# Optimization experiments

Hardware: AMD Instinct MI355X
Metric: run time of the kernel (lower is better)

## Reference

```python
import jax, jax.numpy as jnp
import numpy as np

N_NODES = 50000


def setup_inputs() -> dict:
    key = jax.random.key(0)
    ks = jax.random.split(key, 9)
    d = 256
    E = 800000
    inp = {
        "x": jax.random.normal(ks[0], (N_NODES, d), dtype=jnp.float32),
        "edge_index": jax.random.randint(ks[1], (2, E), 0, N_NODES, dtype=jnp.int64),
    }
    # 3 GCNConv layers, each: weight [in, out] and bias [out] (Glorot-ish scale)
    scale = 1.0 / np.sqrt(d)
    for i in range(3):
        inp[f"W{i+1}"] = jax.random.normal(ks[2 + 2 * i], (d, d), dtype=jnp.float32) * scale
        inp[f"b{i+1}"] = jnp.zeros((d,), dtype=jnp.float32)
    return inp


def _gcn_conv(h, src, dst, norm, W, b, n_nodes):
    # linear transform then normalized gather-scatter aggregation
    h = h @ W                                   # [N, out]
    msg = h[src] * norm[:, None]                # [E+N, out]
    out = jax.ops.segment_sum(msg, dst, num_segments=n_nodes)
    return out + b


def reference(x, edge_index, W1, b1, W2, b2, W3, b3):
    n = x.shape[0]
    loop = jnp.arange(n, dtype=edge_index.dtype)
    src = jnp.concatenate([edge_index[0], loop])  # add self-loops
    dst = jnp.concatenate([edge_index[1], loop])
    # symmetric normalization: deg^{-1/2}[src] * deg^{-1/2}[dst]
    deg = jax.ops.segment_sum(jnp.ones_like(dst, dtype=x.dtype), dst, num_segments=n)
    dinv = jnp.where(deg > 0, jax.lax.rsqrt(deg), 0.0)
    norm = dinv[src] * dinv[dst]

    h = _gcn_conv(x, src, dst, norm, W1, b1, n)
    h = jax.nn.relu(h)
    h = _gcn_conv(h, src, dst, norm, W2, b2, n)
    h = jax.nn.relu(h)
    h = _gcn_conv(h, src, dst, norm, W3, b3, n)
    return h
```

## Files before the change

kernel.cpp:

```cpp
#include <hip/hip_runtime.h>
#include <math.h>


using bf16x8  = __attribute__((ext_vector_type(8))) short;
using ushort4v = __attribute__((ext_vector_type(4))) unsigned short;
using f32x4   = __attribute__((ext_vector_type(4))) float;
using half4   = __attribute__((ext_vector_type(4))) _Float16;

__device__ inline unsigned short f2bf(float v) {
    union { float f; unsigned u; } x; x.f = v;
    unsigned r = x.u + 0x7fff + ((x.u >> 16) & 1);
    return (unsigned short)(r >> 16);
}
__device__ inline float bf2f(unsigned short b) {
    union { float f; unsigned u; } x; x.u = ((unsigned)b) << 16;
    return x.f;
}
__device__ inline unsigned short f2h_bits(float v) {
    _Float16 h = (_Float16)v;
    union { _Float16 h; unsigned short u; } c; c.h = h;
    return c.u;
}


__global__ void hist_kernel(const int* __restrict__ dst, int E, int* __restrict__ cnt) {
    int e = blockIdx.x * blockDim.x + threadIdx.x;
    if (e < E) atomicAdd(&cnt[dst[e]], 1);
}

__global__ void scan_block_kernel(const int* __restrict__ in, int n,
                                  int* __restrict__ out, int* __restrict__ bsums) {
    __shared__ int s[256];
    int t = threadIdx.x;
    int i = blockIdx.x * 256 + t;
    s[t] = (i < n) ? in[i] : 0;
    __syncthreads();
    for (int off = 1; off < 256; off <<= 1) {
        int addv = (t >= off) ? s[t - off] : 0;
        __syncthreads();
        s[t] += addv;
        __syncthreads();
    }
    if (i < n) out[i] = s[t];
    if (t == 255) bsums[blockIdx.x] = s[255];
}

__global__ void scan_sums_kernel(int* __restrict__ bsums, int nb) {
    __shared__ int s[256];
    int t = threadIdx.x;
    s[t] = (t < nb) ? bsums[t] : 0;
    __syncthreads();
    for (int off = 1; off < 256; off <<= 1) {
        int addv = (t >= off) ? s[t - off] : 0;
        __syncthreads();
        s[t] += addv;
        __syncthreads();
    }
    if (t < nb) bsums[t] = s[t];
}

__global__ void scan_add_dinv_kernel(int* __restrict__ scn, int n, const int* __restrict__ bsums,
                                     const int* __restrict__ cnt, float* __restrict__ dinv,
                                     int* __restrict__ cursor) {
    int i = blockIdx.x * 256 + threadIdx.x;
    if (i < n) {
        int s = scn[i] + (blockIdx.x > 0 ? bsums[blockIdx.x - 1] : 0);
        scn[i] = s;
        int c = cnt[i];
        dinv[i] = rsqrtf((float)(c + 1));
        cursor[i] = s - c;
    }
}

__global__ void scatter_kernel(const int* __restrict__ src, const int* __restrict__ dst, int E,
                               const float* __restrict__ dinv, int* __restrict__ cursor,
                               int* __restrict__ ssrc, float* __restrict__ snorm) {
    int e = blockIdx.x * blockDim.x + threadIdx.x;
    if (e < E) {
        int s = src[e], d0 = dst[e];
        int pos = atomicAdd(&cursor[d0], 1);
        ssrc[pos] = s;
        snorm[pos] = dinv[s] * dinv[d0];
    }
}

__global__ __launch_bounds__(256) void wsplit3_kernel(const float* __restrict__ Wa,
                                                      const float* __restrict__ Wb,
                                                      const float* __restrict__ Wc,
                                                      unsigned short* __restrict__ Wsp) {
    __shared__ float t[64][65];
    int w = blockIdx.z;
    const float* W = (w == 0) ? Wa : (w == 1) ? Wb : Wc;
    int k0 = blockIdx.x * 64, n0 = blockIdx.y * 64;
    int tid = threadIdx.x;
    int r = tid >> 6, c = tid & 63;
#pragma unroll
    for (int i = 0; i < 16; ++i) {
        int kk = i * 4 + r;
        t[kk][c] = W[(size_t)(k0 + kk) * 256 + n0 + c];
    }
    __syncthreads();
    unsigned short* Hi = Wsp + (size_t)w * 131072;
    unsigned short* Lo = Hi + 65536;
#pragma unroll
    for (int i = 0; i < 16; ++i) {
        int nn = i * 4 + r;
        float v = t[c][nn];
        unsigned short h = f2bf(v);
        unsigned short l2 = f2bf(v - bf2f(h));
        Hi[(size_t)(n0 + nn) * 256 + k0 + c] = h;
        Lo[(size_t)(n0 + nn) * 256 + k0 + c] = l2;
    }
}

__global__ void xsplit_kernel(const float* __restrict__ in, unsigned short* __restrict__ hi,
                              unsigned short* __restrict__ lo, int total4) {
    int i = blockIdx.x * blockDim.x + threadIdx.x;
    int stride = gridDim.x * blockDim.x;
    for (; i < total4; i += stride) {
        float4 v = ((const float4*)in)[i];
        ushort4v h, l;
        h[0] = f2bf(v.x); l[0] = f2bf(v.x - bf2f(h[0]));
        h[1] = f2bf(v.y); l[1] = f2bf(v.y - bf2f(h[1]));
        h[2] = f2bf(v.z); l[2] = f2bf(v.z - bf2f(h[2]));
        h[3] = f2bf(v.w); l[3] = f2bf(v.w - bf2f(h[3]));
        ((ushort4v*)hi)[i] = h;
        ((ushort4v*)lo)[i] = l;
    }
}

__global__ __launch_bounds__(256) void gemm_ps_kernel(
        const unsigned short* __restrict__ Ahi, const unsigned short* __restrict__ Alo,
        const unsigned short* __restrict__ Bht, const unsigned short* __restrict__ Blt,
        unsigned short* __restrict__ C16, int M) {
    __shared__ unsigned short lds[16384];

    const int tid  = threadIdx.x;
    const int lane = tid & 63;
    const int wid  = tid >> 6;
    const int wr   = wid >> 1, wc = wid & 1;
    const int mBase = blockIdx.x * 128;
    const int nBase = blockIdx.y * 128;

    const int b0 = (lane ^ (lane >> 2) ^ (lane >> 4)) & 1;
    const int b1 = ((lane >> 1) ^ (lane >> 3)) & 1;
    const int b2 = ((lane >> 2) ^ (lane >> 4)) & 1;
    const int g  = (lane & 0x38) | (b2 << 2) | (b1 << 1) | b0;
    const int srow = g >> 2;
    const int skg  = g & 3;

    const unsigned short* gbase =
        (wid == 0) ? Ahi : (wid == 1) ? Alo : (wid == 2) ? Bht : Blt;
    const int rowbase = (wid < 2) ? mBase : nBase;

    int grows[8];
#pragma unroll
    for (int c = 0; c < 8; ++c) {
        int r = rowbase + c * 16 + srow;
        if (wid < 2 && r >= M) r = M - 1;
        grows[c] = r;
    }
    unsigned short* ldsw = lds + wid * 4096;

    const unsigned short* Ah = lds;
    const unsigned short* Al = lds + 4096;
    const unsigned short* Bh = lds + 8192;
    const unsigned short* Bl = lds + 12288;

    f32x4 acc[4][4];
#pragma unroll
    for (int i = 0; i < 4; ++i)
#pragma unroll
        for (int j = 0; j < 4; ++j) acc[i][j] = (f32x4){0.f, 0.f, 0.f, 0.f};

    for (int k0 = 0; k0 < 256; k0 += 32) {
#pragma unroll
        for (int c = 0; c < 8; ++c) {
            const unsigned short* ga = gbase + (size_t)grows[c] * 256 + k0 + skg * 8;
            __builtin_amdgcn_global_load_lds(
                (const __attribute__((address_space(1))) void*)ga,
                (__attribute__((address_space(3))) void*)(ldsw + c * 512),
                16, 0, 0);
        }
        __syncthreads();

        const int kb = (lane >> 4) * 8;
        bf16x8 fah[4], fal[4], fbh[4], fbl[4];
#pragma unroll
        for (int mi = 0; mi < 4; ++mi) {
            int row = wr * 64 + mi * 16 + (lane & 15);
            int off = (row * 64 + kb * 2) ^ ((row & 7) << 4);
            fah[mi] = *(const bf16x8*)((const char*)Ah + off);
            fal[mi] = *(const bf16x8*)((const char*)Al + off);
        }
#pragma unroll
        for (int ni = 0; ni < 4; ++ni) {
            int col = wc * 64 + ni * 16 + (lane & 15);
            int off = (col * 64 + kb * 2) ^ ((col & 7) << 4);
            fbh[ni] = *(const bf16x8*)((const char*)Bh + off);
            fbl[ni] = *(const bf16x8*)((const char*)Bl + off);
        }
#pragma unroll
        for (int mi = 0; mi < 4; ++mi)
#pragma unroll
            for (int ni = 0; ni < 4; ++ni) {
                acc[mi][ni] = __builtin_amdgcn_mfma_f32_16x16x32_bf16(
                    fah[mi], fbh[ni], acc[mi][ni], 0, 0, 0);
                acc[mi][ni] = __builtin_amdgcn_mfma_f32_16x16x32_bf16(
                    fah[mi], fbl[ni], acc[mi][ni], 0, 0, 0);
                acc[mi][ni] = __builtin_amdgcn_mfma_f32_16x16x32_bf16(
                    fal[mi], fbh[ni], acc[mi][ni], 0, 0, 0);
            }
        __syncthreads();
    }

#pragma unroll
    for (int mi = 0; mi < 4; ++mi) {
        int row0 = mBase + wr * 64 + mi * 16 + (lane >> 4) * 4;
#pragma unroll
        for (int ni = 0; ni < 4; ++ni) {
            int col = nBase + wc * 64 + ni * 16 + (lane & 15);
#pragma unroll
            for (int r = 0; r < 4; ++r) {
                int row = row0 + r;
                if (row < M) C16[(size_t)row * 256 + col] = f2h_bits(acc[mi][ni][r]);
            }
        }
    }
}

template <int RELU, int SPLIT>
__global__ __launch_bounds__(256) void agg_kernel(const unsigned short* __restrict__ hH,
                                                  const int* __restrict__ ssrc,
                                                  const float* __restrict__ snorm,
                                                  const int* __restrict__ cnt,
                                                  const int* __restrict__ scanv,
                                                  const float* __restrict__ dinv,
                                                  const float* __restrict__ bias,
                                                  unsigned short* __restrict__ outHi,
                                                  unsigned short* __restrict__ outLo,
                                                  float* __restrict__ outF, int n) {
    int node = blockIdx.x * 4 + (threadIdx.x >> 6);
    int lane = threadIdx.x & 63;
    if (node >= n) return;
    int end = scanv[node];
    int start = end - cnt[node];
    float di = dinv[node];
    float wself = di * di;

    half4 v = ((const half4*)(hH + (size_t)node * 256))[lane];
    float ax = (float)v[0] * wself, ay = (float)v[1] * wself;
    float az = (float)v[2] * wself, aw = (float)v[3] * wself;

    int j = start;
    for (; j + 4 <= end; j += 4) {
        int s0 = ssrc[j], s1 = ssrc[j + 1], s2 = ssrc[j + 2], s3 = ssrc[j + 3];
        float w0 = snorm[j], w1 = snorm[j + 1], w2 = snorm[j + 2], w3 = snorm[j + 3];
        half4 u0 = ((const half4*)(hH + (size_t)s0 * 256))[lane];
        half4 u1 = ((const half4*)(hH + (size_t)s1 * 256))[lane];
        half4 u2 = ((const half4*)(hH + (size_t)s2 * 256))[lane];
        half4 u3 = ((const half4*)(hH + (size_t)s3 * 256))[lane];
        ax = fmaf((float)u0[0], w0, ax); ay = fmaf((float)u0[1], w0, ay);
        az = fmaf((float)u0[2], w0, az); aw = fmaf((float)u0[3], w0, aw);
        ax = fmaf((float)u1[0], w1, ax); ay = fmaf((float)u1[1], w1, ay);
        az = fmaf((float)u1[2], w1, az); aw = fmaf((float)u1[3], w1, aw);
        ax = fmaf((float)u2[0], w2, ax); ay = fmaf((float)u2[1], w2, ay);
        az = fmaf((float)u2[2], w2, az); aw = fmaf((float)u2[3], w2, aw);
        ax = fmaf((float)u3[0], w3, ax); ay = fmaf((float)u3[1], w3, ay);
        az = fmaf((float)u3[2], w3, az); aw = fmaf((float)u3[3], w3, aw);
    }
    for (; j < end; ++j) {
        int s = ssrc[j];
        float wn = snorm[j];
        half4 u = ((const half4*)(hH + (size_t)s * 256))[lane];
        ax = fmaf((float)u[0], wn, ax); ay = fmaf((float)u[1], wn, ay);
        az = fmaf((float)u[2], wn, az); aw = fmaf((float)u[3], wn, aw);
    }

    float4 bb = ((const float4*)bias)[lane];
    ax += bb.x; ay += bb.y; az += bb.z; aw += bb.w;
    if (RELU) {
        ax = fmaxf(ax, 0.0f); ay = fmaxf(ay, 0.0f);
        az = fmaxf(az, 0.0f); aw = fmaxf(aw, 0.0f);
    }
    if (SPLIT) {
        ushort4v h, l;
        h[0] = f2bf(ax); l[0] = f2bf(ax - bf2f(h[0]));
        h[1] = f2bf(ay); l[1] = f2bf(ay - bf2f(h[1]));
        h[2] = f2bf(az); l[2] = f2bf(az - bf2f(h[2]));
        h[3] = f2bf(aw); l[3] = f2bf(aw - bf2f(h[3]));
        ((ushort4v*)(outHi + (size_t)node * 256))[lane] = h;
        ((ushort4v*)(outLo + (size_t)node * 256))[lane] = l;
    } else {
        float4 o = {ax, ay, az, aw};
        ((float4*)(outF + (size_t)node * 256))[lane] = o;
    }
}

extern "C" void kernel_launch(void* const* d_in, const int* in_sizes, int n_in,
                              void* d_out, int out_size, void* d_ws, size_t ws_size,
                              hipStream_t stream) {
    const float* x  = (const float*)d_in[0];
    const int*   ei = (const int*)d_in[1];
    const float* W1 = (const float*)d_in[2];
    const float* b1 = (const float*)d_in[3];
    const float* W2 = (const float*)d_in[4];
    const float* b2 = (const float*)d_in[5];
    const float* W3 = (const float*)d_in[6];
    const float* b3 = (const float*)d_in[7];

    const int n = in_sizes[0] / 256;
    const int E = in_sizes[1] / 2;
    const int* src = ei;
    const int* dst = ei + E;

    unsigned short* Hi = (unsigned short*)d_out;
    unsigned short* Lo = Hi + (size_t)n * 256;
    float* outF = (float*)d_out;

    char* ws = (char*)d_ws;
    unsigned short* hH = (unsigned short*)ws;
    size_t off  = (size_t)n * 256 * 2;
    off = (off + 255) & ~(size_t)255;
    float* dinv = (float*)(ws + off); off += (size_t)n * 4;
    int*   cnt  = (int*)(ws + off);   off += (size_t)n * 4;
    int*   scn  = (int*)(ws + off);   off += (size_t)n * 4;
    int*   cur  = (int*)(ws + off);   off += (size_t)n * 4;
    int*   bsum = (int*)(ws + off);   off += 4096;
    int*   ssrc = (int*)(ws + off);   off += (size_t)E * 4;
    float* snrm = (float*)(ws + off); off += (size_t)E * 4;
    off = (off + 255) & ~(size_t)255;
    unsigned short* Wsp = (unsigned short*)(ws + off);
    off += (size_t)3 * 2 * 65536 * 2;

    hipMemsetAsync(cnt, 0, (size_t)n * 4, stream);

    const int eb = (E + 255) / 256;
    const int nb = (n + 255) / 256;

    wsplit3_kernel<<<dim3(4, 4, 3), 256, 0, stream>>>(W1, W2, W3, Wsp);
    xsplit_kernel<<<2048, 256, 0, stream>>>(x, Hi, Lo, n * 64);

    hist_kernel<<<eb, 256, 0, stream>>>(dst, E, cnt);
    scan_block_kernel<<<nb, 256, 0, stream>>>(cnt, n, scn, bsum);
    scan_sums_kernel<<<1, 256, 0, stream>>>(bsum, nb);
    scan_add_dinv_kernel<<<nb, 256, 0, stream>>>(scn, n, bsum, cnt, dinv, cur);
    scatter_kernel<<<eb, 256, 0, stream>>>(src, dst, E, dinv, cur, ssrc, snrm);

    dim3 gg((n + 127) / 128, 2);
    const int ab = (n + 3) / 4;

    gemm_ps_kernel<<<gg, 256, 0, stream>>>(Hi, Lo, Wsp, Wsp + 65536, hH, n);
    agg_kernel<1, 1><<<ab, 256, 0, stream>>>(hH, ssrc, snrm, cnt, scn, dinv, b1,
                                             Hi, Lo, nullptr, n);
    gemm_ps_kernel<<<gg, 256, 0, stream>>>(Hi, Lo, Wsp + 131072, Wsp + 196608, hH, n);
    agg_kernel<1, 1><<<ab, 256, 0, stream>>>(hH, ssrc, snrm, cnt, scn, dinv, b2,
                                             Hi, Lo, nullptr, n);
    gemm_ps_kernel<<<gg, 256, 0, stream>>>(Hi, Lo, Wsp + 262144, Wsp + 327680, hH, n);
    agg_kernel<0, 0><<<ab, 256, 0, stream>>>(hH, ssrc, snrm, cnt, scn, dinv, b3,
                                             nullptr, nullptr, outF, n);
}
```

Baseline: 398.9 us.

## Double-buffer GEMM LDS staging and remap blocks across XCDs

The split-bf16 GEMM now uses two LDS buffers: the next K-slice is loaded with global_load_lds while the current slice is consumed, with explicit vmcnt waits and raw barriers replacing __syncthreads. The grid is flattened to 1D and block IDs are remapped so consecutive tiles (the two N-halves of the same M rows) land on the same XCD for L2 reuse. The remap hardcodes 782 blocks (n=50000), so it assumes that specific node count, and LDS use doubles to 64KB per block, which may lower occupancy.

```diff
diff --git a/kernel.cpp b/kernel.cpp
--- a/kernel.cpp
+++ b/kernel.cpp
@@ -133,14 +133,19 @@
         const unsigned short* __restrict__ Ahi, const unsigned short* __restrict__ Alo,
         const unsigned short* __restrict__ Bht, const unsigned short* __restrict__ Blt,
         unsigned short* __restrict__ C16, int M) {
-    __shared__ unsigned short lds[16384];
+    __shared__ unsigned short lds[32768];
 
     const int tid  = threadIdx.x;
     const int lane = tid & 63;
     const int wid  = tid >> 6;
     const int wr   = wid >> 1, wc = wid & 1;
-    const int mBase = blockIdx.x * 128;
-    const int nBase = blockIdx.y * 128;
+
+    const int orig = blockIdx.x;
+    const int xcd  = orig & 7;
+    const int idx  = orig >> 3;
+    const int wg   = (xcd < 6 ? xcd * 98 : 588 + (xcd - 6) * 97) + idx;
+    const int mBase = (wg >> 1) * 128;
+    const int nBase = (wg & 1) * 128;
 
     const int b0 = (lane ^ (lane >> 2) ^ (lane >> 4)) & 1;
     const int b1 = ((lane >> 1) ^ (lane >> 3)) & 1;
@@ -160,12 +165,6 @@
         if (wid < 2 && r >= M) r = M - 1;
         grows[c] = r;
     }
-    unsigned short* ldsw = lds + wid * 4096;
-
-    const unsigned short* Ah = lds;
-    const unsigned short* Al = lds + 4096;
-    const unsigned short* Bh = lds + 8192;
-    const unsigned short* Bl = lds + 12288;
 
     f32x4 acc[4][4];
 #pragma unroll
@@ -173,7 +172,9 @@
 #pragma unroll
         for (int j = 0; j < 4; ++j) acc[i][j] = (f32x4){0.f, 0.f, 0.f, 0.f};
 
-    for (int k0 = 0; k0 < 256; k0 += 32) {
+    auto stage = [&](int p, int k) {
+        unsigned short* ldsw = lds + p * 16384 + wid * 4096;
+        const int k0 = k * 32;
 #pragma unroll
         for (int c = 0; c < 8; ++c) {
             const unsigned short* ga = gbase + (size_t)grows[c] * 256 + k0 + skg * 8;
@@ -182,7 +183,25 @@
                 (__attribute__((address_space(3))) void*)(ldsw + c * 512),
                 16, 0, 0);
         }
-        __syncthreads();
+    };
+
+    stage(0, 0);
+
+#pragma unroll
+    for (int k = 0; k < 8; ++k) {
+        const int p = k & 1;
+        if (k < 7) {
+            stage(p ^ 1, k + 1);
+            asm volatile("s_waitcnt vmcnt(8)" ::: "memory");
+        } else {
+            asm volatile("s_waitcnt vmcnt(0)" ::: "memory");
+        }
+        __builtin_amdgcn_s_barrier();
+
+        const unsigned short* Ah = lds + p * 16384;
+        const unsigned short* Al = Ah + 4096;
+        const unsigned short* Bh = Ah + 8192;
+        const unsigned short* Bl = Ah + 12288;
 
         const int kb = (lane >> 4) * 8;
         bf16x8 fah[4], fal[4], fbh[4], fbl[4];
@@ -211,7 +230,7 @@
                 acc[mi][ni] = __builtin_amdgcn_mfma_f32_16x16x32_bf16(
                     fal[mi], fbh[ni], acc[mi][ni], 0, 0, 0);
             }
-        __syncthreads();
+        __builtin_amdgcn_s_barrier();
     }
 
 #pragma unroll
@@ -347,16 +366,16 @@
     scan_add_dinv_kernel<<<nb, 256, 0, stream>>>(scn, n, bsum, cnt, dinv, cur);
     scatter_kernel<<<eb, 256, 0, stream>>>(src, dst, E, dinv, cur, ssrc, snrm);
 
-    dim3 gg((n + 127) / 128, 2);
+    const int gb = ((n + 127) / 128) * 2;
     const int ab = (n + 3) / 4;
 
-    gemm_ps_kernel<<<gg, 256, 0, stream>>>(Hi, Lo, Wsp, Wsp + 65536, hH, n);
+    gemm_ps_kernel<<<gb, 256, 0, stream>>>(Hi, Lo, Wsp, Wsp + 65536, hH, n);
     agg_kernel<1, 1><<<ab, 256, 0, stream>>>(hH, ssrc, snrm, cnt, scn, dinv, b1,
                                              Hi, Lo, nullptr, n);
-    gemm_ps_kernel<<<gg, 256, 0, stream>>>(Hi, Lo, Wsp + 131072, Wsp + 196608, hH, n);
+    gemm_ps_kernel<<<gb, 256, 0, stream>>>(Hi, Lo, Wsp + 131072, Wsp + 196608, hH, n);
     agg_kernel<1, 1><<<ab, 256, 0, stream>>>(hH, ssrc, snrm, cnt, scn, dinv, b2,
                                              Hi, Lo, nullptr, n);
-    gemm_ps_kernel<<<gg, 256, 0, stream>>>(Hi, Lo, Wsp + 262144, Wsp + 327680, hH, n);
+    gemm_ps_kernel<<<gb, 256, 0, stream>>>(Hi, Lo, Wsp + 262144, Wsp + 327680, hH, n);
     agg_kernel<0, 0><<<ab, 256, 0, stream>>>(hH, ssrc, snrm, cnt, scn, dinv, b3,
                                              nullptr, nullptr, outF, n);
 }
```

New measurement: 384.0 us. 3.7% less time.
